# Optimization experiments

Measured on AMD Instinct MI355X. Metric: run time of the kernel, lower is better.

## Reference

```python
import jax, jax.numpy as jnp
import numpy as np

NEG = -1e30  # log-domain 'zero' (safe stand-in for -inf)


def _ctc_loss(logits, labels, label_length, logit_length):
    """Dense-label CTC loss, blank = last class, logits [B,T,C] batch-major.

    Matches tf.nn.ctc_loss(blank_index=-1, logits_time_major=False):
    per-example negative log-likelihood via the standard forward algorithm
    on the blank-extended label sequence of length S = 2L+1.
    """
    B, T, C = logits.shape
    L = labels.shape[1]
    S = 2 * L + 1
    blank = C - 1

    logp = jax.nn.log_softmax(logits, axis=-1)           # [B,T,C]
    lp_t = jnp.moveaxis(logp, 1, 0)                      # [T,B,C]

    # Extended label: blank, l1, blank, l2, ..., blank
    y_ext = jnp.full((B, S), blank, dtype=labels.dtype).at[:, 1::2].set(labels)
    s_idx = jnp.arange(S)
    # s -> s-2 skip allowed iff current symbol is a non-blank differing from s-2
    y_m2 = jnp.pad(y_ext, ((0, 0), (2, 0)), constant_values=blank)[:, :-2]
    skip = (s_idx[None, :] >= 2) & (y_ext != blank) & (y_ext != y_m2)  # [B,S]

    emit0 = jnp.take_along_axis(lp_t[0], y_ext, axis=1)  # [B,S]
    alpha0 = jnp.where(s_idx[None, :] <= 1, emit0, NEG)  # paths start at s=0 or 1

    def step(alpha, lp):
        emit = jnp.take_along_axis(lp, y_ext, axis=1)                      # [B,S]
        a1 = jnp.pad(alpha, ((0, 0), (1, 0)), constant_values=NEG)[:, :-1]  # s-1
        a2 = jnp.pad(alpha, ((0, 0), (2, 0)), constant_values=NEG)[:, :-2]  # s-2
        a2 = jnp.where(skip, a2, NEG)
        new = jnp.logaddexp(jnp.logaddexp(alpha, a1), a2) + emit
        return new, new

    _, alphas = jax.lax.scan(step, alpha0, lp_t[1:])     # [T-1,B,S]
    alphas = jnp.concatenate([alpha0[None], alphas], axis=0)  # [T,B,S]

    b = jnp.arange(B)
    final = alphas[logit_length - 1, b]                  # [B,S] alpha at last frame
    end = 2 * label_length                               # index of final blank
    nll = -jnp.logaddexp(final[b, end], final[b, end - 1])
    return jnp.mean(nll)


def setup_inputs() -> dict:
    key = jax.random.key(0)
    k1, k2, k3 = jax.random.split(key, 3)
    B, T, C, L = 256, 256, 512, 64
    logits = jax.random.normal(k1, (B, T, C), dtype=jnp.float32)
    labels = jax.random.randint(k2, (B, L), 0, C - 1, dtype=jnp.int32)  # never blank
    label_length = jax.random.randint(k3, (B,), 16, L + 1, dtype=jnp.int32)
    logit_length = jnp.full((B,), T, dtype=jnp.int32)
    return {"logits": logits, "labels": labels,
            "label_length": label_length, "logit_length": logit_length}


def reference(logits, labels, label_length, logit_length):
    return _ctc_loss(logits, labels, label_length, logit_length)
```

## Files before the change

### kernel.cpp

```cpp
#include <hip/hip_runtime.h>
#include <math.h>

#define NEGV -1e30f

constexpr int Bc = 256;
constexpr int Tc = 256;
constexpr int Cc = 512;
constexpr int Lc = 64;
constexpr int PW = 8;
constexpr int NPH = Tc / PW;
constexpr float INVLN2 = 1.44269504088896340736f;
constexpr float LN2    = 0.69314718055994530942f;

__device__ __forceinline__ float la2(float a, float b) {
    float m = fmaxf(a, b);
    float d = fabsf(a - b);
    return m + __log2f(exp2f(-d) + 1.0f);
}

__device__ __forceinline__ float lse3(float a, float b, float c) {
    float m = fmaxf(fmaxf(a, b), c);
    return m + __log2f(exp2f(a - m) + exp2f(b - m) + exp2f(c - m));
}

__device__ __forceinline__ float dpp_shr1(float x, float fill) {
    int r = __builtin_amdgcn_update_dpp(__float_as_int(fill), __float_as_int(x),
                                        0x138 , 0xF, 0xF, false);
    return __int_as_float(r);
}

__device__ __forceinline__ float wave_sum_dpp(float v) {
#define DPPADD(ctrl)                                                          \
    v += __int_as_float(__builtin_amdgcn_update_dpp(                          \
        0, __float_as_int(v), (ctrl), 0xF, 0xF, true))
    DPPADD(0x111);
    DPPADD(0x112);
    DPPADD(0x114);
    DPPADD(0x118);
    DPPADD(0x142);
    DPPADD(0x143);
#undef DPPADD
    return __int_as_float(__builtin_amdgcn_readlane(__float_as_int(v), 63));
}

__device__ __forceinline__ void phase_barrier() {
    __builtin_amdgcn_sched_barrier(0);
    asm volatile("s_waitcnt lgkmcnt(0)" ::: "memory");
    __builtin_amdgcn_sched_barrier(0);
    __builtin_amdgcn_s_barrier();
    __builtin_amdgcn_sched_barrier(0);
}

__global__ __launch_bounds__(576) void ctc_k(const float* __restrict__ logits,
                                             const int* __restrict__ labels,
                                             const int* __restrict__ lab_len,
                                             const int* __restrict__ log_len,
                                             float* __restrict__ nll) {
    const int b    = blockIdx.x;
    const int tid  = threadIdx.x;
    const int w    = tid >> 6;
    const int lane = tid & 63;

    __shared__ float em[2][PW][66];

    const float* base = logits + (size_t)b * Tc * Cc;
    const int y = labels[b * Lc + lane];

    float4 c0, c1; float cg;
    if (w < PW) {
        const float4* p0 = (const float4*)(base + (size_t)w * Cc);
        c0 = p0[lane]; c1 = p0[lane + 64];
        cg = base[(size_t)w * Cc + y];
    }

    const int  prevlab = __shfl_up(y, 1, 64);
    const bool skip    = (lane >= 1) && (y != prevlab);
    const int  llm1    = log_len[b] - 1;
    float ae = NEGV, ao = NEGV, ax = NEGV;
    float fe = NEGV, fo = NEGV, fx = NEGV;

    auto step = [&](float em_lv, float em_bv, int t) {
        float po = dpp_shr1(ao, NEGV);
        float nae = la2(ae, po) + em_bv;
        float nao = (skip ? lse3(ao, ae, po)
                          : la2(ao, ae)) + em_lv;
        float nax = la2(ax, ao) + em_bv;
        ae = nae; ao = nao; ax = nax;
        if (t == llm1) { fe = ae; fo = ao; fx = ax; }
    };

    auto consume = [&](int g) {
        const float (*rd)[66] = em[g & 1];
        float el[PW], eb[PW];
#pragma unroll
        for (int r = 0; r < PW; ++r) { el[r] = rd[r][lane]; eb[r] = rd[r][64]; }
        const int t0 = g * PW;
        if (g == 0) {
            ae = (lane == 0) ? eb[0] : NEGV;
            ao = (lane == 0) ? el[0] : NEGV;
            ax = NEGV;
            if (llm1 == 0) { fe = ae; fo = ao; fx = ax; }
#pragma unroll
            for (int r = 1; r < PW; ++r) step(el[r], eb[r], r);
        } else {
#pragma unroll
            for (int r = 0; r < PW; ++r) step(el[r], eb[r], t0 + r);
        }
    };

    for (int p = 0; p < NPH; ++p) {
        if (w < PW) {
            const int t = p * PW + w;
            float4 n0, n1; float ng;
            if (p + 1 < NPH) {
                const float4* q =
                    (const float4*)(base + (size_t)(t + PW) * Cc);
                n0 = q[lane]; n1 = q[lane + 64];
                ng = base[(size_t)(t + PW) * Cc + y];
            }
            float e = __expf(c0.x) + __expf(c0.y) + __expf(c0.z) + __expf(c0.w)
                    + __expf(c1.x) + __expf(c1.y) + __expf(c1.z) + __expf(c1.w);
            float lse2 = __log2f(wave_sum_dpp(e));
            em[p & 1][w][lane] = cg * INVLN2 - lse2;
            if (lane == 63)
                em[p & 1][w][64] = c1.w * INVLN2 - lse2;
            c0 = n0; c1 = n1; cg = ng;
        } else if (p > 0) {
            consume(p - 1);
        }
        phase_barrier();
    }

    if (w == PW) {
        consume(NPH - 1);
        const int L  = lab_len[b];
        float f0 = (L == Lc) ? __shfl(fx, 63, 64) : __shfl(fe, L, 64);
        float f1 = __shfl(fo, L - 1, 64);
        if (lane == 0) nll[b] = -LN2 * la2(f0, f1);
    }
}

__global__ __launch_bounds__(256) void reduce_k(const float* __restrict__ nll,
                                                float* __restrict__ out) {
    int tid = threadIdx.x;
    float v = nll[tid];
#pragma unroll
    for (int o = 32; o; o >>= 1) v += __shfl_xor(v, o, 64);
    __shared__ float pr[4];
    if ((tid & 63) == 0) pr[tid >> 6] = v;
    __syncthreads();
    if (tid == 0) out[0] = (pr[0] + pr[1] + pr[2] + pr[3]) * (1.0f / Bc);
}

extern "C" void kernel_launch(void* const* d_in, const int* in_sizes, int n_in,
                              void* d_out, int out_size, void* d_ws, size_t ws_size,
                              hipStream_t stream) {
    const float* logits  = (const float*)d_in[0];
    const int*   labels  = (const int*)d_in[1];
    const int*   lab_len = (const int*)d_in[2];
    const int*   log_len = (const int*)d_in[3];
    float* out = (float*)d_out;
    float* nll = (float*)d_ws;

    hipLaunchKernelGGL(ctc_k, dim3(Bc), dim3(576), 0, stream,
                       logits, labels, lab_len, log_len, nll);
    hipLaunchKernelGGL(reduce_k, dim3(1), dim3(256), 0, stream, nll, out);
}
```

Measured before the change: 201.6 us.

## Replace lockstep block barriers with LDS done-flags and full-length emission buffer

Producer waves now write emissions for every timestep into a full [T][66] shared buffer and publish progress through per-wave volatile done counters, instead of a double-buffered ring synchronized by a block-wide barrier each phase. The consumer wave polls the counters with s_sleep and runs the alpha recursion as soon as a group is ready, so producers can run ahead without waiting on the serial consumer. Producer prefetch depth grows to two groups ahead. This costs about 67KB of LDS per block, which can limit occupancy. It also relies on LDS ordering via lgkmcnt waits and volatile flags rather than a formal fence.

```diff
diff --git a/kernel.cpp b/kernel.cpp
--- a/kernel.cpp
+++ b/kernel.cpp
@@ -8,7 +8,7 @@
 constexpr int Cc = 512;
 constexpr int Lc = 64;
 constexpr int PW = 8;
-constexpr int NPH = Tc / PW;
+constexpr int NGRP = Tc / PW;
 constexpr float INVLN2 = 1.44269504088896340736f;
 constexpr float LN2    = 0.69314718055994530942f;
 
@@ -43,14 +43,6 @@
     return __int_as_float(__builtin_amdgcn_readlane(__float_as_int(v), 63));
 }
 
-__device__ __forceinline__ void phase_barrier() {
-    __builtin_amdgcn_sched_barrier(0);
-    asm volatile("s_waitcnt lgkmcnt(0)" ::: "memory");
-    __builtin_amdgcn_sched_barrier(0);
-    __builtin_amdgcn_s_barrier();
-    __builtin_amdgcn_sched_barrier(0);
-}
-
 __global__ __launch_bounds__(576) void ctc_k(const float* __restrict__ logits,
                                              const int* __restrict__ labels,
                                              const int* __restrict__ lab_len,
@@ -61,78 +53,92 @@
     const int w    = tid >> 6;
     const int lane = tid & 63;
 
-    __shared__ float em[2][PW][66];
+    __shared__ float em[Tc][66];
+    __shared__ int   done[PW];
+
+    if (tid < PW) done[tid] = 0;
+    __syncthreads();
 
     const float* base = logits + (size_t)b * Tc * Cc;
     const int y = labels[b * Lc + lane];
 
-    float4 c0, c1; float cg;
     if (w < PW) {
-        const float4* p0 = (const float4*)(base + (size_t)w * Cc);
-        c0 = p0[lane]; c1 = p0[lane + 64];
-        cg = base[(size_t)w * Cc + y];
-    }
+        const float* a0r = base + (size_t)w * Cc;
+        const float* a1r = base + (size_t)(w + PW) * Cc;
+        float4 c0 = ((const float4*)a0r)[lane], c1 = ((const float4*)a0r)[lane + 64];
+        float  cg = a0r[y];
+        float4 d0 = ((const float4*)a1r)[lane], d1 = ((const float4*)a1r)[lane + 64];
+        float  dg = a1r[y];
 
-    const int  prevlab = __shfl_up(y, 1, 64);
-    const bool skip    = (lane >= 1) && (y != prevlab);
-    const int  llm1    = log_len[b] - 1;
-    float ae = NEGV, ao = NEGV, ax = NEGV;
-    float fe = NEGV, fo = NEGV, fx = NEGV;
-
-    auto step = [&](float em_lv, float em_bv, int t) {
-        float po = dpp_shr1(ao, NEGV);
-        float nae = la2(ae, po) + em_bv;
-        float nao = (skip ? lse3(ao, ae, po)
-                          : la2(ao, ae)) + em_lv;
-        float nax = la2(ax, ao) + em_bv;
-        ae = nae; ao = nao; ax = nax;
-        if (t == llm1) { fe = ae; fo = ao; fx = ax; }
-    };
-
-    auto consume = [&](int g) {
-        const float (*rd)[66] = em[g & 1];
-        float el[PW], eb[PW];
-#pragma unroll
-        for (int r = 0; r < PW; ++r) { el[r] = rd[r][lane]; eb[r] = rd[r][64]; }
-        const int t0 = g * PW;
-        if (g == 0) {
-            ae = (lane == 0) ? eb[0] : NEGV;
-            ao = (lane == 0) ? el[0] : NEGV;
-            ax = NEGV;
-            if (llm1 == 0) { fe = ae; fo = ao; fx = ax; }
-#pragma unroll
-            for (int r = 1; r < PW; ++r) step(el[r], eb[r], r);
-        } else {
-#pragma unroll
-            for (int r = 0; r < PW; ++r) step(el[r], eb[r], t0 + r);
-        }
-    };
-
-    for (int p = 0; p < NPH; ++p) {
-        if (w < PW) {
-            const int t = p * PW + w;
-            float4 n0, n1; float ng;
-            if (p + 1 < NPH) {
-                const float4* q =
-                    (const float4*)(base + (size_t)(t + PW) * Cc);
-                n0 = q[lane]; n1 = q[lane + 64];
-                ng = base[(size_t)(t + PW) * Cc + y];
+        for (int i = 0; i < NGRP; ++i) {
+            float4 e0, e1; float eg;
+            if (i + 2 < NGRP) {
+                const float* ar = base + (size_t)(w + PW * (i + 2)) * Cc;
+                e0 = ((const float4*)ar)[lane];
+                e1 = ((const float4*)ar)[lane + 64];
+                eg = ar[y];
             }
             float e = __expf(c0.x) + __expf(c0.y) + __expf(c0.z) + __expf(c0.w)
                     + __expf(c1.x) + __expf(c1.y) + __expf(c1.z) + __expf(c1.w);
             float lse2 = __log2f(wave_sum_dpp(e));
-            em[p & 1][w][lane] = cg * INVLN2 - lse2;
+            const int t = w + PW * i;
+            em[t][lane] = cg * INVLN2 - lse2;
             if (lane == 63)
-                em[p & 1][w][64] = c1.w * INVLN2 - lse2;
-            c0 = n0; c1 = n1; cg = ng;
-        } else if (p > 0) {
-            consume(p - 1);
+                em[t][64] = c1.w * INVLN2 - lse2;
+            __builtin_amdgcn_sched_barrier(0);
+            asm volatile("s_waitcnt lgkmcnt(0)" ::: "memory");
+            if (lane == 0) *(volatile int*)&done[w] = i + 1;
+            __builtin_amdgcn_sched_barrier(0);
+            c0 = d0; c1 = d1; cg = dg;
+            d0 = e0; d1 = e1; dg = eg;
         }
-        phase_barrier();
-    }
+    } else {
+        const int  prevlab = __shfl_up(y, 1, 64);
+        const bool skip    = (lane >= 1) && (y != prevlab);
+        const int  llm1    = log_len[b] - 1;
+        float ae = NEGV, ao = NEGV, ax = NEGV;
+        float fe = NEGV, fo = NEGV, fx = NEGV;
 
-    if (w == PW) {
-        consume(NPH - 1);
+        auto step = [&](float em_lv, float em_bv, int t) {
+            float po = dpp_shr1(ao, NEGV);
+            float nae = la2(ae, po) + em_bv;
+            float nao = (skip ? lse3(ao, ae, po)
+                              : la2(ao, ae)) + em_lv;
+            float nax = la2(ax, ao) + em_bv;
+            ae = nae; ao = nao; ax = nax;
+            if (t == llm1) { fe = ae; fo = ao; fx = ax; }
+        };
+
+        for (int g = 0; g < NGRP; ++g) {
+            for (;;) {
+                int mn = 0x7fffffff;
+#pragma unroll
+                for (int pw = 0; pw < PW; ++pw)
+                    mn = min(mn, *(volatile int*)&done[pw]);
+                if (mn > g) break;
+                __builtin_amdgcn_s_sleep(2);
+            }
+            asm volatile("" ::: "memory");
+
+            float el[PW], eb[PW];
+#pragma unroll
+            for (int r = 0; r < PW; ++r) {
+                el[r] = em[PW * g + r][lane];
+                eb[r] = em[PW * g + r][64];
+            }
+            if (g == 0) {
+                ae = (lane == 0) ? eb[0] : NEGV;
+                ao = (lane == 0) ? el[0] : NEGV;
+                ax = NEGV;
+                if (llm1 == 0) { fe = ae; fo = ao; fx = ax; }
+#pragma unroll
+                for (int r = 1; r < PW; ++r) step(el[r], eb[r], r);
+            } else {
+#pragma unroll
+                for (int r = 0; r < PW; ++r) step(el[r], eb[r], PW * g + r);
+            }
+        }
+
         const int L  = lab_len[b];
         float f0 = (L == Lc) ? __shfl(fx, 63, 64) : __shfl(fe, L, 64);
         float f1 = __shfl(fo, L - 1, 64);
```

Result: slower. 207.0 us (+2.7%).

## Deepen logits prefetch to three phases and fuse reduction via cooperative grid sync

Applied to the files above, without the earlier changes.

Producer waves now keep three phases of logit rows in registers instead of one, so each global load has more time to arrive before its softmax is computed. The separate reduce kernel is removed. The CTC kernel is launched cooperatively and, after a grid-wide sync, block 0 sums the per-example losses using atomic acquire loads. This saves a kernel launch but adds a grid barrier and more register pressure in the producer waves.

```diff
diff --git a/kernel.cpp b/kernel.cpp
--- a/kernel.cpp
+++ b/kernel.cpp
@@ -1,5 +1,8 @@
 #include <hip/hip_runtime.h>
+#include <hip/hip_cooperative_groups.h>
 #include <math.h>
+
+namespace cg = cooperative_groups;
 
 #define NEGV -1e30f
 
@@ -55,7 +58,8 @@
                                              const int* __restrict__ labels,
                                              const int* __restrict__ lab_len,
                                              const int* __restrict__ log_len,
-                                             float* __restrict__ nll) {
+                                             float* __restrict__ nll,
+                                             float* __restrict__ out) {
     const int b    = blockIdx.x;
     const int tid  = threadIdx.x;
     const int w    = tid >> 6;
@@ -66,11 +70,18 @@
     const float* base = logits + (size_t)b * Tc * Cc;
     const int y = labels[b * Lc + lane];
 
-    float4 c0, c1; float cg;
+    float4 c0, c1, d0, d1, e0, e1;
+    float  cg, dg, eg;
     if (w < PW) {
-        const float4* p0 = (const float4*)(base + (size_t)w * Cc);
-        c0 = p0[lane]; c1 = p0[lane + 64];
+        const float4* pc = (const float4*)(base + (size_t)w * Cc);
+        const float4* pd = (const float4*)(base + (size_t)(w + PW) * Cc);
+        const float4* pe = (const float4*)(base + (size_t)(w + 2 * PW) * Cc);
+        c0 = pc[lane]; c1 = pc[lane + 64];
+        d0 = pd[lane]; d1 = pd[lane + 64];
+        e0 = pe[lane]; e1 = pe[lane + 64];
         cg = base[(size_t)w * Cc + y];
+        dg = base[(size_t)(w + PW) * Cc + y];
+        eg = base[(size_t)(w + 2 * PW) * Cc + y];
     }
 
     const int  prevlab = __shfl_up(y, 1, 64);
@@ -110,13 +121,12 @@
 
     for (int p = 0; p < NPH; ++p) {
         if (w < PW) {
-            const int t = p * PW + w;
             float4 n0, n1; float ng;
-            if (p + 1 < NPH) {
-                const float4* q =
-                    (const float4*)(base + (size_t)(t + PW) * Cc);
-                n0 = q[lane]; n1 = q[lane + 64];
-                ng = base[(size_t)(t + PW) * Cc + y];
+            if (p + 3 < NPH) {
+                const float* ar = base + (size_t)((p + 3) * PW + w) * Cc;
+                n0 = ((const float4*)ar)[lane];
+                n1 = ((const float4*)ar)[lane + 64];
+                ng = ar[y];
             }
             float e = __expf(c0.x) + __expf(c0.y) + __expf(c0.z) + __expf(c0.w)
                     + __expf(c1.x) + __expf(c1.y) + __expf(c1.z) + __expf(c1.w);
@@ -124,7 +134,9 @@
             em[p & 1][w][lane] = cg * INVLN2 - lse2;
             if (lane == 63)
                 em[p & 1][w][64] = c1.w * INVLN2 - lse2;
-            c0 = n0; c1 = n1; cg = ng;
+            c0 = d0; c1 = d1; cg = dg;
+            d0 = e0; d1 = e1; dg = eg;
+            e0 = n0; e1 = n1; eg = ng;
         } else if (p > 0) {
             consume(p - 1);
         }
@@ -136,20 +148,24 @@
         const int L  = lab_len[b];
         float f0 = (L == Lc) ? __shfl(fx, 63, 64) : __shfl(fe, L, 64);
         float f1 = __shfl(fo, L - 1, 64);
-        if (lane == 0) nll[b] = -LN2 * la2(f0, f1);
+        if (lane == 0) {
+            float res = -LN2 * la2(f0, f1);
+            __hip_atomic_store(&nll[b], res, __ATOMIC_RELEASE,
+                               __HIP_MEMORY_SCOPE_AGENT);
+        }
     }
-}
 
-__global__ __launch_bounds__(256) void reduce_k(const float* __restrict__ nll,
-                                                float* __restrict__ out) {
-    int tid = threadIdx.x;
-    float v = nll[tid];
+    cg::this_grid().sync();
+
+    if (b == 0 && w == 0) {
+        float v = 0.0f;
 #pragma unroll
-    for (int o = 32; o; o >>= 1) v += __shfl_xor(v, o, 64);
-    __shared__ float pr[4];
-    if ((tid & 63) == 0) pr[tid >> 6] = v;
-    __syncthreads();
-    if (tid == 0) out[0] = (pr[0] + pr[1] + pr[2] + pr[3]) * (1.0f / Bc);
+        for (int q = 0; q < 4; ++q)
+            v += __hip_atomic_load(&nll[q * 64 + lane], __ATOMIC_ACQUIRE,
+                                   __HIP_MEMORY_SCOPE_AGENT);
+        float s = wave_sum_dpp(v);
+        if (lane == 0) out[0] = s * (1.0f / Bc);
+    }
 }
 
 extern "C" void kernel_launch(void* const* d_in, const int* in_sizes, int n_in,
@@ -162,7 +178,8 @@
     float* out = (float*)d_out;
     float* nll = (float*)d_ws;
 
-    hipLaunchKernelGGL(ctc_k, dim3(Bc), dim3(576), 0, stream,
-                       logits, labels, lab_len, log_len, nll);
-    hipLaunchKernelGGL(reduce_k, dim3(1), dim3(256), 0, stream, nll, out);
+    void* args[] = {(void*)&logits, (void*)&labels, (void*)&lab_len,
+                    (void*)&log_len, (void*)&nll, (void*)&out};
+    hipLaunchCooperativeKernel((const void*)ctc_k, dim3(Bc), dim3(576),
+                               args, 0, stream);
 }
```

Measured after the change: 251.7 us. 1.25x slower.
